# Kernel tuning notes

Hardware: AMD Instinct MI355X
Metric: run time of the kernel (lower is better)

The kernel has to match this reference:

```python
import jax, jax.numpy as jnp
import numpy as np

NUM_HEADS = 8
NUM_LAYERS = 6
NUM_POINTS = 25
# TrajParamIndex: X=0,Y=1,Z=2,VX=3,VY=4,AX=5,AY=6,YAW=7,LENGTH=8,WIDTH=9,HEIGHT=10


def _unit_cube_points(n=NUM_POINTS):
    m = int(np.sqrt(n))
    lin = np.linspace(-1.0, 1.0, m)
    pts = []
    for dim in range(3):
        for sign in (-1.0, 1.0):
            a, b = np.meshgrid(lin, lin, indexing='ij')
            s = np.full_like(a, sign)
            if dim == 0:
                p = np.stack([s, a, b], -1)
            elif dim == 1:
                p = np.stack([a, s, b], -1)
            else:
                p = np.stack([a, b, s], -1)
            pts.append(p.reshape(-1, 3))
    return jnp.asarray(np.concatenate(pts, 0), jnp.float32)  # [150,3]


def _ln(x, g, b):
    m = x.mean(-1, keepdims=True)
    v = ((x - m) ** 2).mean(-1, keepdims=True)
    return (x - m) / jnp.sqrt(v + 1e-5) * g + b


def _mha(q, k, v, wi, bi, wo, bo):
    E = q.shape[-1]
    d = E // NUM_HEADS
    qq = q @ wi[:E].T + bi[:E]
    kk = k @ wi[E:2 * E].T + bi[E:2 * E]
    vv = v @ wi[2 * E:].T + bi[2 * E:]
    B, S, _ = qq.shape
    Sk = kk.shape[1]
    qh = qq.reshape(B, S, NUM_HEADS, d)
    kh = kk.reshape(B, Sk, NUM_HEADS, d)
    vh = vv.reshape(B, Sk, NUM_HEADS, d)
    att = jnp.einsum('bqhd,bkhd->bhqk', qh, kh) / jnp.sqrt(jnp.float32(d))
    att = jax.nn.softmax(att, axis=-1)
    o = jnp.einsum('bhqk,bkhd->bqhd', att, vh).reshape(B, S, E)
    return o @ wo.T + bo


def _bilinear(feat, uv, valid):
    # feat [B,C,H,W], uv [B,M,2] in [0,1] (u along W), valid [B,M] -> [B,M,C]
    B, C, H, W = feat.shape
    px = uv[..., 0] * (W - 1)
    py = uv[..., 1] * (H - 1)
    x0 = jnp.floor(px)
    y0 = jnp.floor(py)
    wx = px - x0
    wy = py - y0
    x0i = jnp.clip(x0, 0, W - 1).astype(jnp.int32)
    x1i = jnp.clip(x0 + 1, 0, W - 1).astype(jnp.int32)
    y0i = jnp.clip(y0, 0, H - 1).astype(jnp.int32)
    y1i = jnp.clip(y0 + 1, 0, H - 1).astype(jnp.int32)
    flat = feat.reshape(B, C, H * W)
    take = jax.vmap(lambda f, i: f[:, i])  # [C,HW],[M] -> [C,M]
    f00 = take(flat, y0i * W + x0i)
    f01 = take(flat, y0i * W + x1i)
    f10 = take(flat, y1i * W + x0i)
    f11 = take(flat, y1i * W + x1i)
    wxb = wx[:, None, :]
    wyb = wy[:, None, :]
    out = (f00 * (1 - wxb) * (1 - wyb) + f01 * wxb * (1 - wyb)
           + f10 * (1 - wxb) * wyb + f11 * wxb * wyb)
    out = out * valid[:, None, :].astype(out.dtype)
    return out.transpose(0, 2, 1)


def _transform_points(box_pts, tp, ego_t, dt):
    # box_pts [B,N,P,3] local, tp [B,N,11], ego_t [B,4] (x,y,yaw,ts), dt [B]
    yaw = tp[..., 7][..., None]  # [B,N,1]
    c, s = jnp.cos(yaw), jnp.sin(yaw)
    lx, ly, lz = box_pts[..., 0], box_pts[..., 1], box_pts[..., 2]
    rx = lx * c - ly * s
    ry = lx * s + ly * c
    dtb = dt[:, None]  # [B,1]
    cx = tp[..., 0] + tp[..., 3] * dtb + 0.5 * tp[..., 5] * dtb ** 2  # [B,N]
    cy = tp[..., 1] + tp[..., 4] * dtb + 0.5 * tp[..., 6] * dtb ** 2
    cz = tp[..., 2]
    wx = rx + cx[..., None]
    wy = ry + cy[..., None]
    wz = lz + cz[..., None]
    ex = ego_t[:, 0][:, None, None]
    ey = ego_t[:, 1][:, None, None]
    eyaw = ego_t[:, 2][:, None, None]
    pxr = wx - ex
    pyr = wy - ey
    gx = pxr * jnp.cos(eyaw) + pyr * jnp.sin(eyaw)
    gy = -pxr * jnp.sin(eyaw) + pyr * jnp.cos(eyaw)
    return jnp.stack([gx, gy, wz], -1)


def _project(wp, cal):
    # wp [B,N,P,3], cal [B,8] = fx,fy,cx,cy,tx,ty,tz,cam_yaw -> uv in [0,1], valid
    fx, fy, cx0, cy0, tx, ty, tz, cyaw = [cal[:, i][:, None, None] for i in range(8)]
    px = wp[..., 0] - tx
    py = wp[..., 1] - ty
    pz = wp[..., 2] - tz
    fwd = px * jnp.cos(cyaw) + py * jnp.sin(cyaw)
    left = -px * jnp.sin(cyaw) + py * jnp.cos(cyaw)
    zc = fwd
    xc = -left
    yc = -pz
    vz = zc > 0.1
    zs = jnp.maximum(zc, 0.1)
    u = fx * xc / zs + cx0
    v = fy * yc / zs + cy0
    valid = vz & (u >= 0) & (u < 1) & (v >= 0) & (v < 1)
    return jnp.stack([u, v], -1), valid


def _forward(features, calib, ego_states, queries, query_pos,
             traj_w1, traj_b1, traj_w2, traj_b2,
             fm_w1, fm_b1, fm_w2, fm_b2,
             sa_in_w, sa_in_b, sa_out_w, sa_out_b,
             ca_in_w, ca_in_b, ca_out_w, ca_out_b,
             l1_w, l1_b, l2_w, l2_b,
             n1_g, n1_b, n2_g, n2_b, n3_g, n3_b):
    unit = _unit_cube_points()  # [P,3]
    P = unit.shape[0]
    cams, B, T = features.shape[0], features.shape[1], features.shape[2]
    Cf = features.shape[3]
    N = queries.shape[0]

    def traj_head(x):
        return jax.nn.relu(x @ traj_w1.T + traj_b1) @ traj_w2.T + traj_b2

    def feature_mlp(x):
        return jax.nn.relu(x @ fm_w1.T + fm_b1) @ fm_w2.T + fm_b2

    q = jnp.broadcast_to(queries[None], (B, N, queries.shape[1]))
    outputs = []
    for li in range(NUM_LAYERS):
        tp = traj_head(q)  # [B,N,11]
        outputs.append(tp)
        dims = tp[..., 8:11][:, :, None, :]  # [B,N,1,3] (L,W,H)
        box_pts = unit[None, None] * dims  # [B,N,P,3]
        acc = jnp.zeros((B, N, Cf), jnp.float32)
        for t in range(T):
            dt = ego_states[:, t, 3] - ego_states[:, -1, 3]  # [B]
            wp = _transform_points(box_pts, tp, ego_states[:, t], dt)
            for ci in range(cams):
                uv, valid = _project(wp, calib[ci])
                samp = _bilinear(features[ci, :, t], uv.reshape(B, N * P, 2),
                                 valid.reshape(B, N * P))  # [B,N*P,Cf]
                acc = acc + samp.reshape(B, N, P, Cf).sum(axis=2)
        agg = acc / jnp.float32(P * T * cams)
        mem = feature_mlp(agg)  # [B,N,Cf]
        # refine layer li (called without query_pos in decoder forward)
        sa = _mha(q, q, q, sa_in_w[li], sa_in_b[li], sa_out_w[li], sa_out_b[li])
        q = _ln(q + sa, n1_g[li], n1_b[li])
        ca = _mha(q, mem, mem, ca_in_w[li], ca_in_b[li], ca_out_w[li], ca_out_b[li])
        q = _ln(q + ca, n2_g[li], n2_b[li])
        ff = jax.nn.relu(q @ l1_w[li].T + l1_b[li]) @ l2_w[li].T + l2_b[li]
        q = _ln(q + ff, n3_g[li], n3_b[li])
    outputs.append(traj_head(q))
    return jnp.stack(outputs)  # [L+1,B,N,11]


def setup_inputs() -> dict:
    key = jax.random.key(0)
    ks = jax.random.split(key, 32)
    cams, B, T, Cf, H, W = 6, 1, 2, 256, 64, 160
    N, E, Dff, L = 128, 256, 512, NUM_LAYERS

    def rn(k, shape, scale=0.05):
        return jax.random.normal(k, shape, jnp.float32) * scale

    features = jax.random.normal(ks[0], (cams, B, T, Cf, H, W), jnp.float32)
    # calibration: fx,fy,cx,cy,tx,ty,tz,cam_yaw; cameras 8m behind origin along view dir
    cal = np.zeros((cams, B, 8), np.float32)
    for ci in range(cams):
        cyaw = ci * (2 * np.pi / cams)
        cal[ci, :, 0] = 1.2
        cal[ci, :, 1] = 1.6
        cal[ci, :, 2] = 0.5
        cal[ci, :, 3] = 0.5
        cal[ci, :, 4] = -8.0 * np.cos(cyaw)
        cal[ci, :, 5] = -8.0 * np.sin(cyaw)
        cal[ci, :, 6] = -0.5
        cal[ci, :, 7] = cyaw
    calib = jnp.asarray(cal)
    ego = np.zeros((B, T, 4), np.float32)
    for t in range(T):
        ego[:, t, 0] = 0.5 * t
        ego[:, t, 2] = 0.01 * t
        ego[:, t, 3] = 0.1 * t
    ego_states = jnp.asarray(ego)
    return {
        'features': features, 'calib': calib, 'ego_states': ego_states,
        'queries': rn(ks[1], (N, E), 1.0), 'query_pos': rn(ks[2], (N, E), 1.0),
        'traj_w1': rn(ks[3], (Dff, E)), 'traj_b1': jnp.zeros((Dff,), jnp.float32),
        'traj_w2': rn(ks[4], (11, Dff)), 'traj_b2': jnp.zeros((11,), jnp.float32),
        'fm_w1': rn(ks[5], (Dff, E)), 'fm_b1': jnp.zeros((Dff,), jnp.float32),
        'fm_w2': rn(ks[6], (E, Dff)), 'fm_b2': jnp.zeros((E,), jnp.float32),
        'sa_in_w': rn(ks[7], (L, 3 * E, E)), 'sa_in_b': jnp.zeros((L, 3 * E), jnp.float32),
        'sa_out_w': rn(ks[8], (L, E, E)), 'sa_out_b': jnp.zeros((L, E), jnp.float32),
        'ca_in_w': rn(ks[9], (L, 3 * E, E)), 'ca_in_b': jnp.zeros((L, 3 * E), jnp.float32),
        'ca_out_w': rn(ks[10], (L, E, E)), 'ca_out_b': jnp.zeros((L, E), jnp.float32),
        'l1_w': rn(ks[11], (L, Dff, E)), 'l1_b': jnp.zeros((L, Dff), jnp.float32),
        'l2_w': rn(ks[12], (L, E, Dff)), 'l2_b': jnp.zeros((L, E), jnp.float32),
        'n1_g': jnp.ones((L, E), jnp.float32), 'n1_b': jnp.zeros((L, E), jnp.float32),
        'n2_g': jnp.ones((L, E), jnp.float32), 'n2_b': jnp.zeros((L, E), jnp.float32),
        'n3_g': jnp.ones((L, E), jnp.float32), 'n3_b': jnp.zeros((L, E), jnp.float32),
    }


def reference(features, calib, ego_states, queries, query_pos,
              traj_w1, traj_b1, traj_w2, traj_b2,
              fm_w1, fm_b1, fm_w2, fm_b2,
              sa_in_w, sa_in_b, sa_out_w, sa_out_b,
              ca_in_w, ca_in_b, ca_out_w, ca_out_b,
              l1_w, l1_b, l2_w, l2_b,
              n1_g, n1_b, n2_g, n2_b, n3_g, n3_b):
    return _forward(features, calib, ego_states, queries, query_pos,
                    traj_w1, traj_b1, traj_w2, traj_b2,
                    fm_w1, fm_b1, fm_w2, fm_b2,
                    sa_in_w, sa_in_b, sa_out_w, sa_out_b,
                    ca_in_w, ca_in_b, ca_out_w, ca_out_b,
                    l1_w, l1_b, l2_w, l2_b,
                    n1_g, n1_b, n2_g, n2_b, n3_g, n3_b)
```

## Files before the change

kernel.cpp:

```cpp
#include <hip/hip_runtime.h>
#include <stdint.h>

typedef unsigned short u16;

#define DEV static __device__ __forceinline__

DEV float b2f(u16 u){ return __uint_as_float(((uint32_t)u) << 16); }
DEV u16 f2b(float f){ uint32_t x = __float_as_uint(f); return (u16)((x + 0x7fffu + ((x >> 16) & 1u)) >> 16); }
DEV int imin(int a, int b){ return a < b ? a : b; }
DEV int imax(int a, int b){ return a > b ? a : b; }

DEV float ld(const void* p, size_t i, int f32){
  return f32 ? ((const float*)p)[i] : b2f(((const u16*)p)[i]);
}

__device__ float4 g_sawT[6*256*768/4];
__device__ float4 g_sowT[6*256*256/4];
__device__ float4 g_cawT[6*256*768/4];
__device__ float4 g_cowT[6*256*256/4];
__device__ float4 g_l1wT[6*256*512/4];
__device__ float4 g_l2wT[6*512*256/4];
__device__ float4 g_tw1T[256*512/4];
__device__ float4 g_fw1T[256*512/4];
__device__ float4 g_fw2T[512*256/4];

DEV float4* wt_dst(int id){
  switch(id){
    case 0: return g_sawT;
    case 1: return g_sowT;
    case 2: return g_cawT;
    case 3: return g_cowT;
    case 4: return g_l1wT;
    case 5: return g_l2wT;
    case 6: return g_tw1T;
    case 7: return g_fw1T;
    default: return g_fw2T;
  }
}

DEV float dotP(const float* x, const float4* wP, int col, const int N, const int K){
  const float4* p = wP + col;
  const float4* x4 = (const float4*)x;
  float s0=0.f,s1=0.f,s2=0.f,s3=0.f;
  #pragma unroll 8
  for(int k4 = 0; k4 < K/4; k4++){
    float4 w = p[(size_t)k4*N];
    float4 xv = x4[k4];
    s0 += xv.x*w.x; s1 += xv.y*w.y; s2 += xv.z*w.z; s3 += xv.w*w.w;
  }
  return (s0+s1)+(s2+s3);
}

DEV void dot2P(const float* x, const float4* wP, int c0, int c1, const int N,
               float* r0, float* r1){
  const float4* p0 = wP + c0;
  const float4* p1 = wP + c1;
  const float4* x4 = (const float4*)x;
  float a0=0,a1=0,a2=0,a3=0,b0=0,b1=0,b2=0,b3=0;
  #pragma unroll 8
  for(int k4 = 0; k4 < 64; k4++){
    float4 xv = x4[k4];
    float4 w0 = p0[(size_t)k4*N];
    float4 w1 = p1[(size_t)k4*N];
    a0+=xv.x*w0.x; a1+=xv.y*w0.y; a2+=xv.z*w0.z; a3+=xv.w*w0.w;
    b0+=xv.x*w1.x; b1+=xv.y*w1.y; b2+=xv.z*w1.z; b3+=xv.w*w1.w;
  }
  *r0=(a0+a1)+(a2+a3); *r1=(b0+b1)+(b2+b3);
}

DEV void dot3P(const float* x, const float4* wP, int t, float* r0, float* r1, float* r2){
  const float4* p0 = wP + t;
  const float4* p1 = wP + t + 256;
  const float4* p2 = wP + t + 512;
  const float4* x4 = (const float4*)x;
  float a0=0,a1=0,a2=0,a3=0,b0=0,b1=0,b2=0,b3=0,c0=0,c1=0,c2=0,c3=0;
  #pragma unroll 4
  for(int k4 = 0; k4 < 64; k4++){
    float4 xv = x4[k4];
    float4 w0 = p0[(size_t)k4*768];
    float4 w1 = p1[(size_t)k4*768];
    float4 w2 = p2[(size_t)k4*768];
    a0+=xv.x*w0.x; a1+=xv.y*w0.y; a2+=xv.z*w0.z; a3+=xv.w*w0.w;
    b0+=xv.x*w1.x; b1+=xv.y*w1.y; b2+=xv.z*w1.z; b3+=xv.w*w1.w;
    c0+=xv.x*w2.x; c1+=xv.y*w2.y; c2+=xv.z*w2.z; c3+=xv.w*w2.w;
  }
  *r0=(a0+a1)+(a2+a3); *r1=(b0+b1)+(b2+b3); *r2=(c0+c1)+(c2+c3);
}

DEV void kv_store_k(float* kT, int t, int qi, float val){
  int hh = t >> 5, i = t & 31;
  kT[((size_t)(hh*1024 + (i>>2)*128 + qi))*4 + (i&3)] = val;
}
DEV void kv_store_v(float* vP, int t, int qi, float val){
  vP[((size_t)((qi>>2)*256 + t))*4 + (qi&3)] = val;
}

DEV float attn_score(const float* qv, const float* kT, int hh, int k){
  const float4* kp = (const float4*)kT + hh*1024 + k;
  const float4* xq = (const float4*)(qv + hh*32);
  float s0=0.f, s1=0.f;
  #pragma unroll
  for(int i4 = 0; i4 < 8; i4 += 2){
    float4 w0 = kp[i4*128], w1 = kp[(i4+1)*128];
    float4 x0 = xq[i4],     x1 = xq[i4+1];
    s0 += x0.x*w0.x + x0.y*w0.y + x0.z*w0.z + x0.w*w0.w;
    s1 += x1.x*w1.x + x1.y*w1.y + x1.z*w1.z + x1.w*w1.w;
  }
  return s0+s1;
}

DEV float attn_av(const float* s, const float* vP, int hh, int t){
  const float4* vp = (const float4*)vP + t;
  const float4* sp = (const float4*)(s + hh*128);
  float a0=0.f, a1=0.f;
  #pragma unroll 8
  for(int k4 = 0; k4 < 32; k4 += 2){
    float4 w0 = vp[(size_t)k4*256], w1 = vp[(size_t)(k4+1)*256];
    float4 s0 = sp[k4],             s1 = sp[k4+1];
    a0 += s0.x*w0.x + s0.y*w0.y + s0.z*w0.z + s0.w*w0.w;
    a1 += s1.x*w1.x + s1.y*w1.y + s1.z*w1.z + s1.w*w1.w;
  }
  return a0+a1;
}

DEV float bsum256(float v, float* buf){
  int t = threadIdx.x;
  for(int off = 32; off > 0; off >>= 1) v += __shfl_xor(v, off);
  if((t & 63) == 0) buf[t >> 6] = v;
  __syncthreads();
  float r = buf[0] + buf[1] + buf[2] + buf[3];
  __syncthreads();
  return r;
}

DEV float lnorm(float r, const void* g, const void* b, size_t off, float* buf, int f32){
  float m = bsum256(r, buf) * (1.f/256.f);
  float d = r - m;
  float v = bsum256(d*d, buf) * (1.f/256.f);
  return d * rsqrtf(v + 1e-5f) * ld(g, off + threadIdx.x, f32) + ld(b, off + threadIdx.x, f32);
}

DEV void traj_headT(const float* qn, const void* b1, const void* w2, const void* b2,
                    float* hbuf, float* tp, void* out, int slot, int qi, int f32){
  int t = threadIdx.x;
  float h0, h1;
  dot2P(qn, g_tw1T, t, t + 256, 512, &h0, &h1);
  hbuf[t]     = fmaxf(0.f, ld(b1, t, f32)     + h0);
  hbuf[t+256] = fmaxf(0.f, ld(b1, t+256, f32) + h1);
  __syncthreads();
  if(t < 176){
    int o = t >> 4, lane = t & 15;
    float s = 0.f;
    for(int k = lane; k < 512; k += 16) s += hbuf[k] * ld(w2, o*512 + k, f32);
    for(int off = 8; off > 0; off >>= 1) s += __shfl_down(s, off, 16);
    if(lane == 0){
      s += ld(b2, o, f32);
      tp[qi*11 + o] = s;
      int oi = (slot*128 + qi)*11 + o;
      if(f32) ((float*)out)[oi] = s; else ((u16*)out)[oi] = f2b(s);
    }
  }
  __syncthreads();
}

DEV void softmax8(float* s){
  int t = threadIdx.x;
  int hh = t >> 5, lane = t & 31;
  float m = -1e30f;
  for(int k = lane; k < 128; k += 32) m = fmaxf(m, s[hh*128 + k]);
  for(int off = 16; off > 0; off >>= 1) m = fmaxf(m, __shfl_xor(m, off, 32));
  float ss = 0.f;
  for(int k = lane; k < 128; k += 32){
    float e = __expf(s[hh*128 + k] - m);
    s[hh*128 + k] = e; ss += e;
  }
  for(int off = 16; off > 0; off >>= 1) ss += __shfl_xor(ss, off, 32);
  float inv = 1.f / ss;
  for(int k = lane; k < 128; k += 32) s[hh*128 + k] *= inv;
}

__global__ void k_detect(const void* cal, int* flag){
  if(threadIdx.x == 0){
    float a = ((const float*)cal)[0];
    flag[0] = (fabsf(a - 1.2f) < 1e-2f) ? 1 : 0;
  }
}

__global__ __launch_bounds__(256) void k_wt(const void* src, int id, int N, int K, const int* flag){
  int f32 = flag[0];
  float* dst = (float*)wt_dst(id);
  int l = blockIdx.z;
  int nb = blockIdx.x, kb = blockIdx.y;
  __shared__ float tile[64][65];
  int t = threadIdx.x;
  for(int it = 0; it < 16; it++){
    int n = it*4 + (t >> 6);
    int k = t & 63;
    tile[n][k] = ld(src, ((size_t)l*N + nb*64 + n)*K + kb*64 + k, f32);
  }
  __syncthreads();
  int kl = t & 3, nn = (t >> 2) & 15, wv = t >> 6;
  int n_local = wv*16 + nn;
  for(int k4 = 0; k4 < 16; k4++){
    int kcol = k4*4 + kl;
    size_t addr = (size_t)l*K*N + (((size_t)(kb*16 + k4))*N + nb*64 + n_local)*4 + kl;
    dst[addr] = tile[n_local][kcol];
  }
}

__global__ __launch_bounds__(256) void k_tr(const void* feat, u16* FTb, const int* flag){
  int f32 = flag[0];
  int bid = blockIdx.x;
  int cc = bid & 3; int rest = bid >> 2;
  int pch = rest % 160; int e = rest / 160;
  __shared__ float tile[64][65];
  int t = threadIdx.x;
  for(int it = 0; it < 16; it++){
    int c = it*4 + (t >> 6);
    int p = t & 63;
    tile[p][c] = ld(feat, ((size_t)(e*256 + cc*64 + c))*10240 + pch*64 + p, f32);
  }
  __syncthreads();
  for(int it = 0; it < 16; it++){
    int p = it*4 + (t >> 6);
    int c = t & 63;
    FTb[((size_t)(e*10240 + pch*64 + p))*256 + cc*64 + c] = f2b(tile[p][c]);
  }
}

__global__ __launch_bounds__(256, 2) void k_init(const void* queries,
    const void* tb1, const void* tw2, const void* tb2,
    const void* sab, const int* flag,
    float* q, float* tp, float* qrow, float* kTsa, float* vsa, float* acc, void* out){
  __shared__ __align__(16) float qn[256]; __shared__ __align__(16) float hbuf[512];
  int t = threadIdx.x, qi = blockIdx.x;
  int f32 = flag[0];
  float v = ld(queries, qi*256 + t, f32);
  qn[t] = v; q[qi*256 + t] = v;
  __syncthreads();
  traj_headT(qn, tb1, tw2, tb2, hbuf, tp, out, 0, qi, f32);
  float c0, c1, c2;
  dot3P(qn, g_sawT, t, &c0, &c1, &c2);
  qrow[qi*256 + t] = ld(sab, t, f32)       + c0;
  kv_store_k(kTsa, t, qi, ld(sab, t + 256, f32) + c1);
  kv_store_v(vsa,  t, qi, ld(sab, t + 512, f32) + c2);
  acc[qi*256 + t] = 0.f;
}

__global__ __launch_bounds__(256) void k_sample(const u16* FTb, const void* feat, int use_ft,
    const void* cal, const void* ego, const float* tp, float* acc, const int* flag){
  int t = threadIdx.x;
  int f32 = flag[0];
  int ob = (blockIdx.x & 7) * 192 + (blockIdx.x >> 3);
  int qi = ob & 127, e = ob >> 7;
  int ci = e >> 1, tt = e & 1;
  __shared__ float tps[11];
  __shared__ int4  soff[152];
  __shared__ float4 sw[152];
  __shared__ float spx[152], spy[152];
  __shared__ int sval[152];
  if(t < 11) tps[t] = tp[qi*11 + t];
  __syncthreads();
  if(t < 150){
    float dt = ld(ego, tt*4 + 3, f32) - ld(ego, 7, f32);
    int face = t/25, rr = t%25, ii = rr/5, jj = rr%5;
    float av = -1.f + 0.5f*ii, bv = -1.f + 0.5f*jj;
    float sg = (face & 1) ? 1.f : -1.f; int dim = face >> 1;
    float ux = (dim == 0) ? sg : av;
    float uy = (dim == 0) ? av : ((dim == 1) ? sg : bv);
    float uz = (dim == 2) ? sg : bv;
    float lx = ux*tps[8], ly = uy*tps[9], lz = uz*tps[10];
    float yaw = tps[7];
    float cyw = cosf(yaw), syw = sinf(yaw);
    float rx = lx*cyw - ly*syw, ry = lx*syw + ly*cyw;
    float dt2 = 0.5f*dt*dt;
    float cxx = tps[0] + tps[3]*dt + tps[5]*dt2;
    float cyy = tps[1] + tps[4]*dt + tps[6]*dt2;
    float wx = rx + cxx, wy = ry + cyy, wz = lz + tps[2];
    float ex = ld(ego, tt*4, f32), ey = ld(ego, tt*4 + 1, f32), eyaw = ld(ego, tt*4 + 2, f32);
    float ce = cosf(eyaw), se = sinf(eyaw);
    float pxr = wx - ex, pyr = wy - ey;
    float gx = pxr*ce + pyr*se, gy = -pxr*se + pyr*ce;
    float fx = ld(cal, ci*8, f32),   fy = ld(cal, ci*8+1, f32);
    float cx0 = ld(cal, ci*8+2, f32), cy0 = ld(cal, ci*8+3, f32);
    float tx = ld(cal, ci*8+4, f32), ty = ld(cal, ci*8+5, f32);
    float tz = ld(cal, ci*8+6, f32), cw = ld(cal, ci*8+7, f32);
    float cc = cosf(cw), sc = sinf(cw);
    float pxc = gx - tx, pyc = gy - ty, pzc = wz - tz;
    float zc = pxc*cc + pyc*sc;
    float left = -pxc*sc + pyc*cc;
    float xc = -left, yc = -pzc;
    float zs = fmaxf(zc, 0.1f);
    float u = fx*xc/zs + cx0, vv = fy*yc/zs + cy0;
    bool val = (zc > 0.1f) && (u >= 0.f) && (u < 1.f) && (vv >= 0.f) && (vv < 1.f);
    float px = u*159.f, py = vv*63.f;
    spx[t] = px; spy[t] = py;
    float x0f = floorf(px), y0f = floorf(py);
    float wxf = px - x0f, wyf = py - y0f;
    int x0 = imin(imax((int)x0f, 0), 159), y0 = imin(imax((int)y0f, 0), 63);
    int x1 = imin(x0 + 1, 159), y1 = imin(y0 + 1, 63);
    soff[t] = make_int4((y0*160 + x0)*256, (y0*160 + x1)*256,
                        (y1*160 + x0)*256, (y1*160 + x1)*256);
    sw[t] = make_float4((1.f-wxf)*(1.f-wyf), wxf*(1.f-wyf), (1.f-wxf)*wyf, wxf*wyf);
    sval[t] = val ? 1 : 0;
  }
  __syncthreads();
  float a = 0.f;
  if(use_ft){
    const u16* base = FTb + (size_t)e*10240*256 + t;
    for(int p = 0; p < 150; p++){
      if(!sval[p]) continue;
      int4 o = soff[p]; float4 w = sw[p];
      a += w.x*b2f(base[o.x]) + w.y*b2f(base[o.y])
         + w.z*b2f(base[o.z]) + w.w*b2f(base[o.w]);
    }
  } else {
    size_t pc = ((size_t)e*256 + t)*10240;
    for(int p = 0; p < 150; p++){
      if(!sval[p]) continue;
      float px = spx[p], py = spy[p];
      float x0f = floorf(px), y0f = floorf(py);
      float wxf = px - x0f, wyf = py - y0f;
      int x0 = imin(imax((int)x0f, 0), 159), y0 = imin(imax((int)y0f, 0), 63);
      int x1 = imin(x0 + 1, 159), y1 = imin(y0 + 1, 63);
      float w00 = (1.f-wxf)*(1.f-wyf), w01 = wxf*(1.f-wyf), w10 = (1.f-wxf)*wyf, w11 = wxf*wyf;
      a += w00*ld(feat, pc + y0*160 + x0, f32) + w01*ld(feat, pc + y0*160 + x1, f32)
         + w10*ld(feat, pc + y1*160 + x0, f32) + w11*ld(feat, pc + y1*160 + x1, f32);
    }
  }
  atomicAdd(&acc[qi*256 + t], a);
}

__global__ __launch_bounds__(256, 2) void k_mksa(const float* acc, const float* q, const float* qrow,
    const float* kTsa, const float* vsa,
    const void* fb1, const void* fb2, const void* cab,
    const void* sob, const void* n1g, const void* n1b,
    int li, float* kvK, float* kvV, float* qs, float* qq, const int* flag){
  __shared__ __align__(16) float xa[256];
  __shared__ __align__(16) float s[1024];
  __shared__ __align__(16) float h[512];
  __shared__ float buf[8];
  int t = threadIdx.x;
  int f32 = flag[0];
  if(blockIdx.x < 128){
    int qi = blockIdx.x;
    xa[t] = acc[qi*256 + t] * (1.f/1800.f);
    __syncthreads();
    float h0, h1;
    dot2P(xa, g_fw1T, t, t + 256, 512, &h0, &h1);
    h[t]     = fmaxf(0.f, ld(fb1, t, f32)     + h0);
    h[t+256] = fmaxf(0.f, ld(fb1, t+256, f32) + h1);
    __syncthreads();
    float m = ld(fb2, t, f32) + dotP(h, g_fw2T, t, 256, 512);
    __syncthreads();
    xa[t] = m;
    __syncthreads();
    const float4* cawT = g_cawT + (size_t)li*49152;
    float kk, vv;
    dot2P(xa, cawT, 256 + t, 512 + t, 768, &kk, &vv);
    size_t bo = (size_t)li*768;
    kv_store_k(kvK, t, qi, ld(cab, bo + 256 + t, f32) + kk);
    kv_store_v(kvV, t, qi, ld(cab, bo + 512 + t, f32) + vv);
  } else {
    int qi = blockIdx.x - 128;
    xa[t] = qrow[qi*256 + t];
    __syncthreads();
    for(int rep = 0; rep < 4; rep++){
      int idx = t + rep*256; int hh = idx >> 7, k = idx & 127;
      s[idx] = attn_score(xa, kTsa, hh, k) * 0.1767766952966369f;
    }
    __syncthreads();
    softmax8(s);
    __syncthreads();
    h[t] = attn_av(s, vsa, t >> 5, t);
    __syncthreads();
    float pr = ld(sob, (size_t)li*256 + t, f32) + dotP(h, g_sowT + (size_t)li*16384, t, 256, 256);
    float r = q[qi*256 + t] + pr;
    float y = lnorm(r, n1g, n1b, (size_t)li*256, buf, f32);
    qs[qi*256 + t] = y;
    __syncthreads();
    xa[t] = y;
    __syncthreads();
    qq[qi*256 + t] = ld(cab, (size_t)li*768 + t, f32)
                   + dotP(xa, g_cawT + (size_t)li*49152, t, 768, 256);
  }
}

__global__ __launch_bounds__(256, 2) void k_ca(const float* qs, const float* qq,
    const float* kvK, const float* kvV,
    const void* cob, const void* n2g, const void* n2b,
    const void* l1b, const void* l2b, const void* n3g, const void* n3b,
    const void* tb1, const void* tw2, const void* tb2, const void* sab,
    int li, int have_next,
    float* qout, float* qrow, float* kTsa, float* vsa,
    float* tp, float* acc, void* out, const int* flag){
  __shared__ __align__(16) float qv[256]; __shared__ __align__(16) float s[1024];
  __shared__ __align__(16) float o[256];  __shared__ __align__(16) float q2[256];
  __shared__ __align__(16) float h[512];  __shared__ float buf[8];
  int t = threadIdx.x, qi = blockIdx.x;
  int f32 = flag[0];
  qv[t] = qq[qi*256 + t];
  __syncthreads();
  for(int rep = 0; rep < 4; rep++){
    int idx = t + rep*256; int hh = idx >> 7, k = idx & 127;
    s[idx] = attn_score(qv, kvK, hh, k) * 0.1767766952966369f;
  }
  __syncthreads();
  softmax8(s);
  __syncthreads();
  o[t] = attn_av(s, kvV, t >> 5, t);
  __syncthreads();
  float pr = ld(cob, (size_t)li*256 + t, f32) + dotP(o, g_cowT + (size_t)li*16384, t, 256, 256);
  float r = qs[qi*256 + t] + pr;
  float y = lnorm(r, n2g, n2b, (size_t)li*256, buf, f32);
  q2[t] = y;
  __syncthreads();
  float h0, h1;
  dot2P(q2, g_l1wT + (size_t)li*32768, t, t + 256, 512, &h0, &h1);
  h[t]     = fmaxf(0.f, ld(l1b, (size_t)li*512 + t, f32)     + h0);
  h[t+256] = fmaxf(0.f, ld(l1b, (size_t)li*512 + t+256, f32) + h1);
  __syncthreads();
  float ff = ld(l2b, (size_t)li*256 + t, f32) + dotP(h, g_l2wT + (size_t)li*32768, t, 256, 512);
  float r3 = q2[t] + ff;
  float y3 = lnorm(r3, n3g, n3b, (size_t)li*256, buf, f32);
  qout[qi*256 + t] = y3;
  __syncthreads();
  q2[t] = y3;
  __syncthreads();
  traj_headT(q2, tb1, tw2, tb2, h, tp, out, li + 1, qi, f32);
  if(have_next){
    float c0, c1, c2;
    dot3P(q2, g_sawT + (size_t)(li+1)*49152, t, &c0, &c1, &c2);
    size_t sb = (size_t)(li+1)*768;
    qrow[qi*256 + t] = ld(sab, sb + t, f32) + c0;
    kv_store_k(kTsa, t, qi, ld(sab, sb + 256 + t, f32) + c1);
    kv_store_v(vsa,  t, qi, ld(sab, sb + 512 + t, f32) + c2);
  }
  acc[qi*256 + t] = 0.f;
}

extern "C" void kernel_launch(void* const* d_in, const int* in_sizes, int n_in,
                              void* d_out, int out_size, void* d_ws, size_t ws_size,
                              hipStream_t stream){
  const void* feat    = d_in[0];
  const void* calib   = d_in[1];
  const void* ego     = d_in[2];
  const void* queries = d_in[3];
  const void* tw1 = d_in[5];  const void* tb1 = d_in[6];
  const void* tw2 = d_in[7];  const void* tb2 = d_in[8];
  const void* fw1 = d_in[9];  const void* fb1 = d_in[10];
  const void* fw2 = d_in[11]; const void* fb2 = d_in[12];
  const void* saw = d_in[13]; const void* sab = d_in[14];
  const void* sow = d_in[15]; const void* sob = d_in[16];
  const void* caw = d_in[17]; const void* cab = d_in[18];
  const void* cow = d_in[19]; const void* cob = d_in[20];
  const void* l1w = d_in[21]; const void* l1b = d_in[22];
  const void* l2w = d_in[23]; const void* l2b = d_in[24];
  const void* n1g = d_in[25]; const void* n1b = d_in[26];
  const void* n2g = d_in[27]; const void* n2b = d_in[28];
  const void* n3g = d_in[29]; const void* n3b = d_in[30];

  float* ws   = (float*)d_ws;
  int*   flag = (int*)d_ws;
  float* q    = ws + 16;
  float* qs   = ws + 32784;
  float* tp   = ws + 65552;
  float* qrow = ws + 67088;
  float* kTsa = ws + 99856;
  float* vsa  = ws + 132624;
  float* kvK  = ws + 165392;
  float* kvV  = ws + 198160;
  float* qq   = ws + 230928;
  float* acc  = ws + 263696;
  u16*   FTb  = (u16*)(ws + 296464);
  size_t need = (size_t)296464*4 + (size_t)12*10240*256*2;
  int use_ft = (ws_size >= need) ? 1 : 0;

  k_detect<<<1, 64, 0, stream>>>(calib, flag);

  k_wt<<<dim3(12, 4, 6), 256, 0, stream>>>(saw, 0, 768, 256, flag);
  k_wt<<<dim3( 4, 4, 6), 256, 0, stream>>>(sow, 1, 256, 256, flag);
  k_wt<<<dim3(12, 4, 6), 256, 0, stream>>>(caw, 2, 768, 256, flag);
  k_wt<<<dim3( 4, 4, 6), 256, 0, stream>>>(cow, 3, 256, 256, flag);
  k_wt<<<dim3( 8, 4, 6), 256, 0, stream>>>(l1w, 4, 512, 256, flag);
  k_wt<<<dim3( 4, 8, 6), 256, 0, stream>>>(l2w, 5, 256, 512, flag);
  k_wt<<<dim3( 8, 4, 1), 256, 0, stream>>>(tw1, 6, 512, 256, flag);
  k_wt<<<dim3( 8, 4, 1), 256, 0, stream>>>(fw1, 7, 512, 256, flag);
  k_wt<<<dim3( 4, 8, 1), 256, 0, stream>>>(fw2, 8, 256, 512, flag);

  if(use_ft) k_tr<<<12*160*4, 256, 0, stream>>>(feat, FTb, flag);
  k_init<<<128, 256, 0, stream>>>(queries, tb1, tw2, tb2, sab, flag,
                                  q, tp, qrow, kTsa, vsa, acc, d_out);
  for(int li = 0; li < 6; li++){
    k_sample<<<1536, 256, 0, stream>>>(FTb, feat, use_ft, calib, ego, tp, acc, flag);
    k_mksa<<<256, 256, 0, stream>>>(acc, q, qrow, kTsa, vsa, fb1, fb2, cab,
                                    sob, n1g, n1b, li, kvK, kvV, qs, qq, flag);
    int hn = (li < 5) ? 1 : 0;
    k_ca<<<128, 256, 0, stream>>>(qs, qq, kvK, kvV, cob, n2g, n2b,
                                  l1b, l2b, n3g, n3b,
                                  tb1, tw2, tb2, sab, li, hn,
                                  q, qrow, kTsa, vsa, tp, acc, d_out, flag);
  }
  (void)in_sizes; (void)n_in; (void)out_size;
}
```

Measured before the change: 1.140 ms.

## Merge self-attention blocks into sampling kernel and compact valid sample points

The self-attention branch, which depends only on the previous layer's outputs, moves from the post-sampling kernel into extra blocks of the sampling kernel, so it overlaps with feature sampling and the later kernel only runs the feature MLP and K/V projection. The sampling loop now iterates over a compacted list of valid points built with a shared atomic and unrolls by four to issue more independent gathers. The transpose kernel writes pairs of bf16 values per store. Costs include heavier per-block shared memory and a 2-blocks-per-SM launch bound on the sampling kernel, which may limit occupancy, and accumulation order now depends on the atomic list order.

```diff
diff --git a/kernel.cpp b/kernel.cpp
--- a/kernel.cpp
+++ b/kernel.cpp
@@ -221,10 +221,12 @@
     tile[p][c] = ld(feat, ((size_t)(e*256 + cc*64 + c))*10240 + pch*64 + p, f32);
   }
   __syncthreads();
-  for(int it = 0; it < 16; it++){
-    int p = it*4 + (t >> 6);
-    int c = t & 63;
-    FTb[((size_t)(e*10240 + pch*64 + p))*256 + cc*64 + c] = f2b(tile[p][c]);
+  for(int it = 0; it < 8; it++){
+    int p = it*8 + (t >> 5);
+    int c = (t & 31)*2;
+    ushort2 v;
+    v.x = f2b(tile[p][c]); v.y = f2b(tile[p][c+1]);
+    *(ushort2*)&FTb[((size_t)(e*10240 + pch*64 + p))*256 + cc*64 + c] = v;
   }
 }
 
@@ -247,18 +249,55 @@
   acc[qi*256 + t] = 0.f;
 }
 
-__global__ __launch_bounds__(256) void k_sample(const u16* FTb, const void* feat, int use_ft,
-    const void* cal, const void* ego, const float* tp, float* acc, const int* flag){
+__global__ __launch_bounds__(256, 2) void k_samsa(const u16* FTb, const void* feat, int use_ft,
+    const void* cal, const void* ego, const float* tp, float* acc,
+    const float* q, const float* qrow, const float* kTsa, const float* vsa,
+    const void* sob, const void* n1g, const void* n1b, const void* cab,
+    int li, float* qs, float* qq, const int* flag){
   int t = threadIdx.x;
   int f32 = flag[0];
-  int ob = (blockIdx.x & 7) * 192 + (blockIdx.x >> 3);
-  int qi = ob & 127, e = ob >> 7;
-  int ci = e >> 1, tt = e & 1;
+  __shared__ __align__(16) float xa[256];
+  __shared__ __align__(16) float s[1024];
+  __shared__ __align__(16) float h[512];
+  __shared__ float buf[8];
   __shared__ float tps[11];
   __shared__ int4  soff[152];
   __shared__ float4 sw[152];
   __shared__ float spx[152], spy[152];
   __shared__ int sval[152];
+  __shared__ int plist[152];
+  __shared__ int pcnt;
+
+  if(blockIdx.x < 128){
+    int qi = blockIdx.x;
+    xa[t] = qrow[qi*256 + t];
+    __syncthreads();
+    for(int rep = 0; rep < 4; rep++){
+      int idx = t + rep*256; int hh = idx >> 7, k = idx & 127;
+      s[idx] = attn_score(xa, kTsa, hh, k) * 0.1767766952966369f;
+    }
+    __syncthreads();
+    softmax8(s);
+    __syncthreads();
+    h[t] = attn_av(s, vsa, t >> 5, t);
+    __syncthreads();
+    float pr = ld(sob, (size_t)li*256 + t, f32) + dotP(h, g_sowT + (size_t)li*16384, t, 256, 256);
+    float r = q[qi*256 + t] + pr;
+    float y = lnorm(r, n1g, n1b, (size_t)li*256, buf, f32);
+    qs[qi*256 + t] = y;
+    __syncthreads();
+    xa[t] = y;
+    __syncthreads();
+    qq[qi*256 + t] = ld(cab, (size_t)li*768 + t, f32)
+                   + dotP(xa, g_cawT + (size_t)li*49152, t, 768, 256);
+    return;
+  }
+
+  int sb = blockIdx.x - 128;
+  int ob = (sb & 7) * 192 + (sb >> 3);
+  int qi = ob & 127, e = ob >> 7;
+  int ci = e >> 1, tt = e & 1;
+  if(t == 0) pcnt = 0;
   if(t < 11) tps[t] = tp[qi*11 + t];
   __syncthreads();
   if(t < 150){
@@ -303,13 +342,29 @@
                         (y1*160 + x0)*256, (y1*160 + x1)*256);
     sw[t] = make_float4((1.f-wxf)*(1.f-wyf), wxf*(1.f-wyf), (1.f-wxf)*wyf, wxf*wyf);
     sval[t] = val ? 1 : 0;
+    if(val){ int ix = atomicAdd(&pcnt, 1); plist[ix] = t; }
   }
   __syncthreads();
   float a = 0.f;
   if(use_ft){
     const u16* base = FTb + (size_t)e*10240*256 + t;
-    for(int p = 0; p < 150; p++){
-      if(!sval[p]) continue;
+    int np = pcnt;
+    int pp = 0;
+    for(; pp + 4 <= np; pp += 4){
+      int p0 = plist[pp], p1 = plist[pp+1], p2 = plist[pp+2], p3 = plist[pp+3];
+      int4 o0 = soff[p0]; int4 o1 = soff[p1]; int4 o2 = soff[p2]; int4 o3 = soff[p3];
+      float4 w0 = sw[p0]; float4 w1 = sw[p1]; float4 w2 = sw[p2]; float4 w3 = sw[p3];
+      float v00 = b2f(base[o0.x]), v01 = b2f(base[o0.y]), v02 = b2f(base[o0.z]), v03 = b2f(base[o0.w]);
+      float v10 = b2f(base[o1.x]), v11 = b2f(base[o1.y]), v12 = b2f(base[o1.z]), v13 = b2f(base[o1.w]);
+      float v20 = b2f(base[o2.x]), v21 = b2f(base[o2.y]), v22 = b2f(base[o2.z]), v23 = b2f(base[o2.w]);
+      float v30 = b2f(base[o3.x]), v31 = b2f(base[o3.y]), v32 = b2f(base[o3.z]), v33 = b2f(base[o3.w]);
+      a += w0.x*v00 + w0.y*v01 + w0.z*v02 + w0.w*v03;
+      a += w1.x*v10 + w1.y*v11 + w1.z*v12 + w1.w*v13;
+      a += w2.x*v20 + w2.y*v21 + w2.z*v22 + w2.w*v23;
+      a += w3.x*v30 + w3.y*v31 + w3.z*v32 + w3.w*v33;
+    }
+    for(; pp < np; pp++){
+      int p = plist[pp];
       int4 o = soff[p]; float4 w = sw[p];
       a += w.x*b2f(base[o.x]) + w.y*b2f(base[o.y])
          + w.z*b2f(base[o.z]) + w.w*b2f(base[o.w]);
@@ -331,59 +386,30 @@
   atomicAdd(&acc[qi*256 + t], a);
 }
 
-__global__ __launch_bounds__(256, 2) void k_mksa(const float* acc, const float* q, const float* qrow,
-    const float* kTsa, const float* vsa,
+__global__ __launch_bounds__(256, 2) void k_mk(const float* acc,
     const void* fb1, const void* fb2, const void* cab,
-    const void* sob, const void* n1g, const void* n1b,
-    int li, float* kvK, float* kvV, float* qs, float* qq, const int* flag){
+    int li, float* kvK, float* kvV, const int* flag){
   __shared__ __align__(16) float xa[256];
-  __shared__ __align__(16) float s[1024];
   __shared__ __align__(16) float h[512];
-  __shared__ float buf[8];
-  int t = threadIdx.x;
+  int t = threadIdx.x, qi = blockIdx.x;
   int f32 = flag[0];
-  if(blockIdx.x < 128){
-    int qi = blockIdx.x;
-    xa[t] = acc[qi*256 + t] * (1.f/1800.f);
-    __syncthreads();
-    float h0, h1;
-    dot2P(xa, g_fw1T, t, t + 256, 512, &h0, &h1);
-    h[t]     = fmaxf(0.f, ld(fb1, t, f32)     + h0);
-    h[t+256] = fmaxf(0.f, ld(fb1, t+256, f32) + h1);
-    __syncthreads();
-    float m = ld(fb2, t, f32) + dotP(h, g_fw2T, t, 256, 512);
-    __syncthreads();
-    xa[t] = m;
-    __syncthreads();
-    const float4* cawT = g_cawT + (size_t)li*49152;
-    float kk, vv;
-    dot2P(xa, cawT, 256 + t, 512 + t, 768, &kk, &vv);
-    size_t bo = (size_t)li*768;
-    kv_store_k(kvK, t, qi, ld(cab, bo + 256 + t, f32) + kk);
-    kv_store_v(kvV, t, qi, ld(cab, bo + 512 + t, f32) + vv);
-  } else {
-    int qi = blockIdx.x - 128;
-    xa[t] = qrow[qi*256 + t];
-    __syncthreads();
-    for(int rep = 0; rep < 4; rep++){
-      int idx = t + rep*256; int hh = idx >> 7, k = idx & 127;
-      s[idx] = attn_score(xa, kTsa, hh, k) * 0.1767766952966369f;
-    }
-    __syncthreads();
-    softmax8(s);
-    __syncthreads();
-    h[t] = attn_av(s, vsa, t >> 5, t);
-    __syncthreads();
-    float pr = ld(sob, (size_t)li*256 + t, f32) + dotP(h, g_sowT + (size_t)li*16384, t, 256, 256);
-    float r = q[qi*256 + t] + pr;
-    float y = lnorm(r, n1g, n1b, (size_t)li*256, buf, f32);
-    qs[qi*256 + t] = y;
-    __syncthreads();
-    xa[t] = y;
-    __syncthreads();
-    qq[qi*256 + t] = ld(cab, (size_t)li*768 + t, f32)
-                   + dotP(xa, g_cawT + (size_t)li*49152, t, 768, 256);
-  }
+  xa[t] = acc[qi*256 + t] * (1.f/1800.f);
+  __syncthreads();
+  float h0, h1;
+  dot2P(xa, g_fw1T, t, t + 256, 512, &h0, &h1);
+  h[t]     = fmaxf(0.f, ld(fb1, t, f32)     + h0);
+  h[t+256] = fmaxf(0.f, ld(fb1, t+256, f32) + h1);
+  __syncthreads();
+  float m = ld(fb2, t, f32) + dotP(h, g_fw2T, t, 256, 512);
+  __syncthreads();
+  xa[t] = m;
+  __syncthreads();
+  const float4* cawT = g_cawT + (size_t)li*49152;
+  float kk, vv;
+  dot2P(xa, cawT, 256 + t, 512 + t, 768, &kk, &vv);
+  size_t bo = (size_t)li*768;
+  kv_store_k(kvK, t, qi, ld(cab, bo + 256 + t, f32) + kk);
+  kv_store_v(kvV, t, qi, ld(cab, bo + 512 + t, f32) + vv);
 }
 
 __global__ __launch_bounds__(256, 2) void k_ca(const float* qs, const float* qq,
@@ -492,9 +518,10 @@
   k_init<<<128, 256, 0, stream>>>(queries, tb1, tw2, tb2, sab, flag,
                                   q, tp, qrow, kTsa, vsa, acc, d_out);
   for(int li = 0; li < 6; li++){
-    k_sample<<<1536, 256, 0, stream>>>(FTb, feat, use_ft, calib, ego, tp, acc, flag);
-    k_mksa<<<256, 256, 0, stream>>>(acc, q, qrow, kTsa, vsa, fb1, fb2, cab,
-                                    sob, n1g, n1b, li, kvK, kvV, qs, qq, flag);
+    k_samsa<<<1664, 256, 0, stream>>>(FTb, feat, use_ft, calib, ego, tp, acc,
+                                      q, qrow, kTsa, vsa, sob, n1g, n1b, cab,
+                                      li, qs, qq, flag);
+    k_mk<<<128, 256, 0, stream>>>(acc, fb1, fb2, cab, li, kvK, kvV, flag);
     int hn = (li < 5) ? 1 : 0;
     k_ca<<<128, 256, 0, stream>>>(qs, qq, kvK, kvV, cob, n2g, n2b,
                                   l1b, l2b, n3g, n3b,
```

Result: faster. 1.116 ms (-2.0%).
